# Optimization experiments

Measured on AMD Instinct MI355X. Metric: run time of the kernel, lower is better.

Reference implementation:

```python
import jax, jax.numpy as jnp
import numpy as np

N_ITERS = 100   # fixed ADMM (OSQP-style) iteration count
RHO = 1.0       # ADMM penalty
SIGMA = 1e-6    # OSQP regularization


def setup_inputs() -> dict:
    key = jax.random.key(0)
    ks = jax.random.split(key, 12)
    B, S, H, nA = 16384, 512, 1024, 24
    mEq, mIneq = 4, 8
    state = jax.random.normal(ks[0], (B, S), dtype=jnp.float32)
    Aeq = jax.random.normal(ks[1], (mEq, nA), dtype=jnp.float32)
    beq = jax.random.normal(ks[2], (mEq,), dtype=jnp.float32)
    A = jax.random.normal(ks[3], (mIneq, nA), dtype=jnp.float32)
    b = jax.random.uniform(ks[4], (mIneq,), dtype=jnp.float32)
    ub = jnp.ones((nA,), dtype=jnp.float32)
    lb = jnp.zeros((nA,), dtype=jnp.float32)
    # MLP parameters (3 Dense layers as in the flax module)
    W1 = jax.random.normal(ks[5], (S, H), dtype=jnp.float32) / np.sqrt(S).astype(np.float32)
    b1 = jnp.zeros((H,), dtype=jnp.float32)
    W2 = jax.random.normal(ks[6], (H, H), dtype=jnp.float32) / np.sqrt(H).astype(np.float32)
    b2 = jnp.zeros((H,), dtype=jnp.float32)
    W3 = jax.random.normal(ks[7], (H, nA), dtype=jnp.float32) / np.sqrt(H).astype(np.float32)
    b3 = jnp.zeros((nA,), dtype=jnp.float32)
    return dict(state=state, Aeq=Aeq, beq=beq, A=A, b=b, ub=ub, lb=lb,
                W1=W1, b1=b1, W2=W2, b2=b2, W3=W3, b3=b3)


def reference(state, Aeq, beq, A, b, ub, lb, W1, b1, W2, b2, W3, b3):
    # ---- 3-layer MLP ----
    h = jax.nn.relu(state @ W1 + b1)
    h = jax.nn.relu(h @ W2 + b2)
    raw = h @ W3 + b3                      # [B, n]
    n = raw.shape[-1]
    I = jnp.eye(n, dtype=raw.dtype)
    # ---- stack constraints exactly as solve_qp: [Aeq; A_ineq; I; -I] ----
    A_tot = jnp.concatenate([Aeq, A, I, -I], axis=0)            # [M, n]
    neg_inf = jnp.full((A.shape[0],), -jnp.inf, dtype=raw.dtype)
    l_tot = jnp.concatenate([beq, neg_inf, lb, -ub])            # [M]
    u_tot = jnp.concatenate([beq, b, ub, -lb])                  # [M]
    # ---- OSQP-style ADMM: min 0.5||x||^2 - raw'x  s.t. l <= A_tot x <= u ----
    q = -raw                                                    # [B, n]
    M = (1.0 + SIGMA) * I + RHO * (A_tot.T @ A_tot)             # [n, n] (P = I)
    Minv = jnp.linalg.inv(M)
    B_, m = q.shape[0], A_tot.shape[0]
    X0 = jnp.zeros_like(q)
    Z0 = jnp.zeros((B_, m), dtype=q.dtype)
    Y0 = jnp.zeros((B_, m), dtype=q.dtype)

    def step(carry, _):
        X, Z, Y = carry
        rhs = SIGMA * X - q + (RHO * Z - Y) @ A_tot             # [B, n]
        Xn = rhs @ Minv.T                                       # [B, n]
        Zt = Xn @ A_tot.T                                       # [B, m]
        Zn = jnp.clip(Zt + Y / RHO, l_tot, u_tot)
        Yn = Y + RHO * (Zt - Zn)
        return (Xn, Zn, Yn), None

    (X, Z, Y), _ = jax.lax.scan(step, (X0, Z0, Y0), None, length=N_ITERS)
    return X
```

## Files before the change

### kernel.cpp

```cpp
#include <hip/hip_runtime.h>

using uint = unsigned int;
using ushort = unsigned short;

typedef __attribute__((ext_vector_type(8))) short bf16x8;
typedef __attribute__((ext_vector_type(4))) float f32x4;

#define ADMM_ITERS 100
#define RHO_C 1.0f
#define SIGMA_C 1e-6f

__device__ inline ushort f2bf(float f) {
  union { float f; uint u; } c; c.f = f;
  uint u = c.u;
  uint r = (u + 0x7fffu + ((u >> 16) & 1u)) >> 16;
  return (ushort)r;
}

__device__ inline void gload_lds16(const void* g, void* l) {
  __builtin_amdgcn_global_load_lds(
      (const __attribute__((address_space(1))) void*)g,
      (__attribute__((address_space(3))) void*)l, 16, 0, 0);
}

__device__ inline void splitPack(const float* x, bf16x8& hi, bf16x8& lo) {
#pragma unroll
  for (int j = 0; j < 8; ++j) {
    uint b = __float_as_uint(x[j]);
    uint hb = b & 0xffff0000u;
    float lf = x[j] - __uint_as_float(hb);
    hi[j] = (short)(b >> 16);
    lo[j] = (short)(__float_as_uint(lf) >> 16);
  }
}

__global__ void convert_bf16(const float* __restrict__ in, ushort* __restrict__ out, int n4) {
  int i = blockIdx.x * blockDim.x + threadIdx.x;
  if (i >= n4) return;
  float4 v = ((const float4*)in)[i];
  uint2 p;
  p.x = (uint)f2bf(v.x) | ((uint)f2bf(v.y) << 16);
  p.y = (uint)f2bf(v.z) | ((uint)f2bf(v.w) << 16);
  ((uint2*)out)[i] = p;
}

__global__ void transpose_f32_bf16(const float* __restrict__ in, ushort* __restrict__ out,
                                   int R, int C, int Cout) {
  __shared__ float t[32][33];
  const int c0 = blockIdx.x * 32, r0 = blockIdx.y * 32;
  const int tx = threadIdx.x & 31, ty = threadIdx.x >> 5;
  for (int rr = ty; rr < 32; rr += 8) {
    int r = r0 + rr, c = c0 + tx;
    float v = 0.0f;
    if (r < R && c < C) v = in[(long)r * C + c];
    t[rr][tx] = v;
  }
  __syncthreads();
  for (int rr = ty; rr < 32; rr += 8) {
    int c = c0 + rr, r = r0 + tx;
    if (c < Cout && r < R) out[(long)c * R + r] = f2bf(t[tx][rr]);
  }
}

__global__ void setup_admm(const float* __restrict__ Aeq, const float* __restrict__ beq,
                           const float* __restrict__ A, const float* __restrict__ b,
                           const float* __restrict__ ub, const float* __restrict__ lb,
                           ushort* __restrict__ Th, ushort* __restrict__ Tl,
                           ushort* __restrict__ T0h, ushort* __restrict__ T0l,
                           float* __restrict__ blp, float* __restrict__ bup) {
  __shared__ float Aug[24][48];
  __shared__ float A12[12 * 24];
  __shared__ float fac[24];
  __shared__ float Tx[24][36];
  const int t = threadIdx.x;
  for (int i = t; i < 48 * 64; i += 256) { Th[i] = 0; Tl[i] = 0; }
  for (int i = t; i < 48 * 32; i += 256) { T0h[i] = 0; T0l[i] = 0; }
  if (t < 96)  A12[t] = Aeq[t];
  if (t < 192) A12[96 + t] = A[t];
  __syncthreads();
  for (int idx = t; idx < 576; idx += 256) {
    int j = idx / 24, k = idx % 24;
    float s = (j == k) ? (1.0f + SIGMA_C + 2.0f * RHO_C) : 0.0f;
    for (int r = 0; r < 12; ++r) s += RHO_C * A12[r * 24 + j] * A12[r * 24 + k];
    Aug[j][k] = s;
    Aug[j][24 + k] = (j == k) ? 1.0f : 0.0f;
  }
  __syncthreads();
  for (int p = 0; p < 24; ++p) {
    float rp = 1.0f / Aug[p][p];
    if (t < 24) fac[t] = Aug[t][p];
    __syncthreads();
    if (t < 48) Aug[p][t] *= rp;
    __syncthreads();
    for (int idx = t; idx < 24 * 48; idx += 256) {
      int r = idx / 48, c = idx % 48;
      if (r != p) Aug[r][c] -= fac[r] * Aug[p][c];
    }
    __syncthreads();
  }
  auto splitStore = [](ushort* hp, ushort* lp, int i, float v) {
    ushort hs = f2bf(v);
    float hf = __uint_as_float(((uint)hs) << 16);
    ushort ls = f2bf(v - hf);
    hp[i] = hs; lp[i] = ls;
  };
  for (int idx = t; idx < 24 * 36; idx += 256) {
    int n = idx / 36, k = idx % 36;
    float v;
    if (k < 24) v = 2.0f * Aug[n][24 + k];
    else {
      v = 0.0f;
      for (int j = 0; j < 24; ++j) v += Aug[n][24 + j] * A12[(k - 24) * 24 + j];
    }
    Tx[n][k] = v;
    splitStore(Th, Tl, n * 64 + k, v);
  }
  __syncthreads();
  for (int idx = t; idx < 12 * 36; idx += 256) {
    int m = idx / 36, k = idx % 36;
    float v = 0.0f;
    for (int j = 0; j < 24; ++j) v += A12[m * 24 + j] * Tx[j][k];
    splitStore(Th, Tl, (24 + m) * 64 + k, v);
  }
  for (int idx = t; idx < 36 * 24; idx += 256) {
    int n = idx / 24, k = idx % 24;
    float v;
    if (n < 24) v = Aug[n][24 + k];
    else {
      v = 0.0f;
      for (int j = 0; j < 24; ++j) v += A12[(n - 24) * 24 + j] * Aug[j][24 + k];
    }
    splitStore(T0h, T0l, n * 32 + k, v);
  }
  if (t < 48) {
    float lv, uv;
    if (t < 24)      { lv = lb[t]; uv = ub[t]; }
    else if (t < 28) { lv = beq[t - 24]; uv = lv; }
    else if (t < 36) { lv = -1e30f; uv = b[t - 28]; }
    else             { lv = -1e30f; uv = 1e30f; }
    blp[t] = lv; bup[t] = uv;
  }
}

template<int BM, int BN, int WM, int WN, int TM, int TN, int MODE>
__global__ __launch_bounds__(256) void gemm_bt(
    const ushort* __restrict__ A, const ushort* __restrict__ Bt,
    const float* __restrict__ bias, void* __restrict__ Cout_,
    int K, int ldc, int nvalid) {
  __shared__ char lds[(BM + BN) * 64];
  char* ldsA = lds;
  char* ldsB = lds + BM * 64;

  const int tid = threadIdx.x;
  const int wave = tid >> 6;
  const int lane = tid & 63;
  const int blockM = blockIdx.y * BM;
  const int blockN = blockIdx.x * BN;
  const int wm = (wave / WN) * (TM * 16);
  const int wn = (wave % WN) * (TN * 16);

  f32x4 acc[TM][TN] = {};

  const int l15 = lane & 15;
  const int kq = lane >> 4;
  constexpr int AI = BM / 16;
  constexpr int TOT = (BM + BN) / 16;
  const int srow = lane >> 2;
  const int kb = (lane & 3) ^ ((srow >> 1) & 3);

  for (int k0 = 0; k0 < K; k0 += 32) {
    for (int inst = wave; inst < TOT; inst += 4) {
      const bool isA = inst < AI;
      const int i = isA ? inst : inst - AI;
      const ushort* gp = (isA ? A : Bt)
          + (long)((isA ? blockM : blockN) + i * 16 + srow) * K + (k0 + kb * 8);
      char* lp = (isA ? ldsA : ldsB) + i * 1024;
      gload_lds16(gp, lp);
    }
    __syncthreads();

    bf16x8 af[TM], bfr[TN];
#pragma unroll
    for (int i = 0; i < TM; ++i) {
      int r = wm + i * 16 + l15;
      int ch = kq ^ ((r >> 1) & 3);
      af[i] = *(const bf16x8*)(ldsA + r * 64 + ch * 16);
    }
#pragma unroll
    for (int j = 0; j < TN; ++j) {
      int r = wn + j * 16 + l15;
      int ch = kq ^ ((r >> 1) & 3);
      bfr[j] = *(const bf16x8*)(ldsB + r * 64 + ch * 16);
    }
#pragma unroll
    for (int i = 0; i < TM; ++i)
#pragma unroll
      for (int j = 0; j < TN; ++j)
        acc[i][j] = __builtin_amdgcn_mfma_f32_16x16x32_bf16(af[i], bfr[j], acc[i][j], 0, 0, 0);
    __syncthreads();
  }

  const int ro = lane >> 4;
#pragma unroll
  for (int i = 0; i < TM; ++i) {
#pragma unroll
    for (int j = 0; j < TN; ++j) {
      const int col = blockN + wn + j * 16 + l15;
      float bv;
      if (MODE == 0) bv = bias[col];
      else bv = (col < nvalid) ? bias[col] : 0.0f;
#pragma unroll
      for (int r = 0; r < 4; ++r) {
        const int row = blockM + wm + i * 16 + ro * 4 + r;
        float v = acc[i][j][r] + bv;
        if (MODE == 0) {
          v = fmaxf(v, 0.0f);
          ((ushort*)Cout_)[(long)row * ldc + col] = f2bf(v);
        } else {
          if (col < nvalid) ((float*)Cout_)[(long)row * ldc + col] = v;
        }
      }
    }
  }
}

__global__ __launch_bounds__(256) void admm_mfma(
    const float* raw,
    const ushort* __restrict__ Th, const ushort* __restrict__ Tl,
    const ushort* __restrict__ T0h, const ushort* __restrict__ T0l,
    const float* __restrict__ blp, const float* __restrict__ bup,
    float* outp) {
  __shared__ __align__(16) float Ubuf[4][16][68];
  const int tid = threadIdx.x, wave = tid >> 6, lane = tid & 63;
  const int l15 = lane & 15, q = lane >> 4;
  const long rowbase = (long)blockIdx.x * 64 + wave * 16;
  float (*U)[68] = Ubuf[wave];

  for (int idx = lane; idx < 256; idx += 64)
    U[idx >> 4][48 + (idx & 15)] = 0.0f;

  float bl[3], bu[3];
#pragma unroll
  for (int t = 0; t < 3; ++t) { bl[t] = blp[16 * t + l15]; bu[t] = bup[16 * t + l15]; }

  f32x4 W[3], base[3];
  {
    bf16x8 t0h[3], t0l[3];
#pragma unroll
    for (int t = 0; t < 3; ++t) {
      t0h[t] = *(const bf16x8*)(T0h + (16 * t + l15) * 32 + q * 8);
      t0l[t] = *(const bf16x8*)(T0l + (16 * t + l15) * 32 + q * 8);
    }
    float qa[8];
    if (q < 3) {
      const float* rp = raw + (rowbase + l15) * 24 + q * 8;
      float4 v0 = *(const float4*)rp;
      float4 v1 = *(const float4*)(rp + 4);
      qa[0] = v0.x; qa[1] = v0.y; qa[2] = v0.z; qa[3] = v0.w;
      qa[4] = v1.x; qa[5] = v1.y; qa[6] = v1.z; qa[7] = v1.w;
    } else {
#pragma unroll
      for (int j = 0; j < 8; ++j) qa[j] = 0.0f;
    }
    bf16x8 qhi, qlo;
    splitPack(qa, qhi, qlo);
#pragma unroll
    for (int t = 0; t < 3; ++t) {
      f32x4 acc = {0.0f, 0.0f, 0.0f, 0.0f};
      acc = __builtin_amdgcn_mfma_f32_16x16x32_bf16(qhi, t0h[t], acc, 0, 0, 0);
      acc = __builtin_amdgcn_mfma_f32_16x16x32_bf16(qlo, t0h[t], acc, 0, 0, 0);
      acc = __builtin_amdgcn_mfma_f32_16x16x32_bf16(qhi, t0l[t], acc, 0, 0, 0);
      base[t] = acc; W[t] = acc;
    }
  }

  bf16x8 tbh[2][3], tbl[2][3];
#pragma unroll
  for (int c = 0; c < 2; ++c)
#pragma unroll
    for (int t = 0; t < 3; ++t) {
      tbh[c][t] = *(const bf16x8*)(Th + (16 * t + l15) * 64 + 32 * c + q * 8);
      tbl[c][t] = *(const bf16x8*)(Tl + (16 * t + l15) * 64 + 32 * c + q * 8);
    }

  float yb0[4], yb1[4];
#pragma unroll 1
  for (int it = 1; it < ADMM_ITERS; ++it) {
    f32x4 C[3];
#pragma unroll
    for (int t = 0; t < 3; ++t) {
#pragma unroll
      for (int r = 0; r < 4; ++r) {
        float w = W[t][r];
        float z = fminf(fmaxf(w, bl[t]), bu[t]);
        float u = 2.0f * z - w;
        float y = w - z;
        C[t][r] = base[t][r] + y;
        if (t == 0) yb0[r] = y;
        if (t == 1) yb1[r] = y;
        U[q * 4 + r][16 * t + l15] = u;
      }
    }
    bf16x8 uh[2], ul[2];
#pragma unroll
    for (int c = 0; c < 2; ++c) {
      const float* up = &U[l15][32 * c + q * 8];
      float4 a0 = *(const float4*)up;
      float4 a1 = *(const float4*)(up + 4);
      float ua[8] = {a0.x, a0.y, a0.z, a0.w, a1.x, a1.y, a1.z, a1.w};
      splitPack(ua, uh[c], ul[c]);
    }
#pragma unroll
    for (int t = 0; t < 3; ++t) {
      f32x4 acc = C[t];
#pragma unroll
      for (int c = 0; c < 2; ++c) {
        acc = __builtin_amdgcn_mfma_f32_16x16x32_bf16(uh[c], tbh[c][t], acc, 0, 0, 0);
        acc = __builtin_amdgcn_mfma_f32_16x16x32_bf16(ul[c], tbh[c][t], acc, 0, 0, 0);
        acc = __builtin_amdgcn_mfma_f32_16x16x32_bf16(uh[c], tbl[c][t], acc, 0, 0, 0);
      }
      W[t] = acc;
    }
  }

#pragma unroll
  for (int r = 0; r < 4; ++r) {
    const long row = rowbase + q * 4 + r;
    outp[row * 24 + l15] = W[0][r] - yb0[r];
    if (l15 < 8) outp[row * 24 + 16 + l15] = W[1][r] - yb1[r];
  }
}

extern "C" void kernel_launch(void* const* d_in, const int* in_sizes, int n_in,
                              void* d_out, int out_size, void* d_ws, size_t ws_size,
                              hipStream_t stream) {
  const float* state = (const float*)d_in[0];
  const float* Aeq   = (const float*)d_in[1];
  const float* beq   = (const float*)d_in[2];
  const float* Ain   = (const float*)d_in[3];
  const float* bin   = (const float*)d_in[4];
  const float* ub    = (const float*)d_in[5];
  const float* lb    = (const float*)d_in[6];
  const float* W1    = (const float*)d_in[7];
  const float* b1    = (const float*)d_in[8];
  const float* W2    = (const float*)d_in[9];
  const float* b2    = (const float*)d_in[10];
  const float* W3    = (const float*)d_in[11];
  const float* b3    = (const float*)d_in[12];

  const int Bn = in_sizes[0] / 512;
  char* ws = (char*)d_ws;
  ushort* stateB = (ushort*)(ws + 0);
  ushort* W1T    = (ushort*)(ws + 16777216);
  ushort* W2T    = (ushort*)(ws + 17825792);
  ushort* W3T    = (ushort*)(ws + 19922944);
  ushort* Th     = (ushort*)(ws + 19993600);
  ushort* Tl     = (ushort*)(ws + 19999744);
  ushort* T0h    = (ushort*)(ws + 20005888);
  ushort* T0l    = (ushort*)(ws + 20008960);
  float*  blp    = (float*) (ws + 20012032);
  float*  bup    = (float*) (ws + 20012224);
  ushort* H1     = (ushort*)(ws + 21565440);
  ushort* H2     = (ushort*)(ws + 55119872);
  float*  rawb   = (float*)d_out;

  const int n4 = (Bn * 512) / 4;
  convert_bf16<<<(n4 + 255) / 256, 256, 0, stream>>>(state, stateB, n4);
  transpose_f32_bf16<<<dim3(32, 16), 256, 0, stream>>>(W1, W1T, 512, 1024, 1024);
  transpose_f32_bf16<<<dim3(32, 32), 256, 0, stream>>>(W2, W2T, 1024, 1024, 1024);
  transpose_f32_bf16<<<dim3(1, 32),  256, 0, stream>>>(W3, W3T, 1024, 24, 32);
  setup_admm<<<1, 256, 0, stream>>>(Aeq, beq, Ain, bin, ub, lb,
                                    Th, Tl, T0h, T0l, blp, bup);

  gemm_bt<128, 128, 2, 2, 4, 4, 0><<<dim3(8, Bn / 128), 256, 0, stream>>>(
      stateB, W1T, b1, H1, 512, 1024, 1024);
  gemm_bt<128, 128, 2, 2, 4, 4, 0><<<dim3(8, Bn / 128), 256, 0, stream>>>(
      H1, W2T, b2, H2, 1024, 1024, 1024);
  gemm_bt<64, 32, 4, 1, 1, 2, 1><<<dim3(1, Bn / 64), 256, 0, stream>>>(
      H2, W3T, b3, rawb, 1024, 24, 24);

  admm_mfma<<<Bn / 64, 256, 0, stream>>>(rawb, Th, Tl, T0h, T0l, blp, bup,
                                         (float*)d_out);
}
```

Baseline: 294.9 us.

## Replace MLP layer GEMMs with 256x256-tile 8-wave pipelined MFMA kernel

Adds a new GEMM kernel for the first two MLP layers. It uses 256x256 output tiles with 8 waves, double-buffered LDS staging through global_load_lds, an XOR swizzle to avoid bank conflicts, and an XCD-aware block-index remap. The K loop is split into four phases that interleave LDS fragment reads, prefetch of the next K tile, and MFMA quads, using barriers and s_setprio to keep the matrix units busy. The goal is more data reuse per tile and better overlap of memory loads with compute. In exchange it needs 128KB of LDS per workgroup and many accumulator registers, which limits occupancy.

```diff
diff --git a/kernel.cpp b/kernel.cpp
--- a/kernel.cpp
+++ b/kernel.cpp
@@ -224,6 +224,136 @@
   }
 }
 
+#define GEMM8P_QUAD(MI0, NJ0)                                                 \
+  _Pragma("unroll") for (int mi_ = 0; mi_ < 4; ++mi_)                         \
+  _Pragma("unroll") for (int nj_ = 0; nj_ < 2; ++nj_)                         \
+  _Pragma("unroll") for (int kk_ = 0; kk_ < 2; ++kk_)                         \
+    acc[(MI0) + mi_][(NJ0) + nj_] = __builtin_amdgcn_mfma_f32_16x16x32_bf16(  \
+        aF[mi_][kk_], bF[(NJ0) + nj_][kk_], acc[(MI0) + mi_][(NJ0) + nj_],    \
+        0, 0, 0);
+
+#define GEMM8P_SYNC_PRE()                              \
+  __builtin_amdgcn_s_barrier();                        \
+  asm volatile("s_waitcnt lgkmcnt(0)" ::: "memory");   \
+  __builtin_amdgcn_sched_barrier(0);                   \
+  __builtin_amdgcn_s_setprio(1);
+
+#define GEMM8P_SYNC_POST()                             \
+  __builtin_amdgcn_s_setprio(0);                       \
+  __builtin_amdgcn_s_barrier();
+
+__global__ __launch_bounds__(512, 2) void gemm8p(
+    const ushort* __restrict__ A, const ushort* __restrict__ Bt,
+    const float* __restrict__ bias, ushort* __restrict__ Cout,
+    int K, int ldc, int nblk_n) {
+  __shared__ __align__(16) char ldsc[131072];
+
+  const int nwg = gridDim.x;
+  const int bid = blockIdx.x;
+  const int swz = (bid & 7) * (nwg >> 3) + (bid >> 3);
+  const int blockM = (swz / nblk_n) * 256;
+  const int blockN = (swz % nblk_n) * 256;
+
+  const int tid = threadIdx.x;
+  const int wave = tid >> 6;
+  const int lane = tid & 63;
+  const int l15 = lane & 15;
+  const int q = lane >> 4;
+  const int wm = (wave >> 2) * 128;
+  const int wn = (wave & 3) * 64;
+  const int nt = K >> 6;
+
+  f32x4 acc[8][4] = {};
+
+  auto stage = [&](int ts, int h) {
+    if (ts >= nt) return;
+    char* base = ldsc + ((ts & 1) << 16) + (h << 14);
+#pragma unroll
+    for (int j = 0; j < 2; ++j) {
+      const int idx = wave * 64 + j * 512 + lane;
+      const int row = idx >> 3;
+      const int cs = (idx & 7) ^ (row & 7);
+      const ushort* gp =
+          (h < 2 ? A + (long)(blockM + ((h & 1) << 7) + row) * K
+                 : Bt + (long)(blockN + ((h & 1) << 7) + row) * K)
+          + (ts << 6) + cs * 8;
+      gload_lds16(gp, base + ((wave * 64 + j * 512) << 4));
+    }
+  };
+  auto dsA = [&](int cb, int mi, int kk) {
+    const int r = wm + mi * 16 + l15;
+    const int cs = (kk * 4 + q) ^ (r & 7);
+    return *(const bf16x8*)(ldsc + (cb << 16) + r * 128 + cs * 16);
+  };
+  auto dsB = [&](int cb, int nj, int kk) {
+    const int r = wn + nj * 16 + l15;
+    const int cs = (kk * 4 + q) ^ (r & 7);
+    return *(const bf16x8*)(ldsc + (cb << 16) + 32768 + r * 128 + cs * 16);
+  };
+
+  stage(0, 0); stage(0, 1); stage(0, 2); stage(0, 3);
+  stage(1, 0);
+  asm volatile("s_waitcnt vmcnt(2)" ::: "memory");
+  __builtin_amdgcn_s_barrier();
+
+  bf16x8 aF[4][2], bF[4][2];
+#pragma unroll 1
+  for (int t = 0; t < nt; ++t) {
+    const int cb = t & 1;
+#pragma unroll
+    for (int mi = 0; mi < 4; ++mi)
+#pragma unroll
+      for (int kk = 0; kk < 2; ++kk) aF[mi][kk] = dsA(cb, mi, kk);
+#pragma unroll
+    for (int nj = 0; nj < 2; ++nj)
+#pragma unroll
+      for (int kk = 0; kk < 2; ++kk) bF[nj][kk] = dsB(cb, nj, kk);
+    stage(t + 1, 1);
+    GEMM8P_SYNC_PRE();
+    GEMM8P_QUAD(0, 0);
+    GEMM8P_SYNC_POST();
+#pragma unroll
+    for (int nj = 2; nj < 4; ++nj)
+#pragma unroll
+      for (int kk = 0; kk < 2; ++kk) bF[nj][kk] = dsB(cb, nj, kk);
+    stage(t + 1, 2);
+    GEMM8P_SYNC_PRE();
+    GEMM8P_QUAD(0, 2);
+    GEMM8P_SYNC_POST();
+#pragma unroll
+    for (int mi = 0; mi < 4; ++mi)
+#pragma unroll
+      for (int kk = 0; kk < 2; ++kk) aF[mi][kk] = dsA(cb, 4 + mi, kk);
+    stage(t + 1, 3);
+    GEMM8P_SYNC_PRE();
+    GEMM8P_QUAD(4, 2);
+    GEMM8P_SYNC_POST();
+    stage(t + 2, 0);
+    if (t + 2 < nt) { asm volatile("s_waitcnt vmcnt(2)" ::: "memory"); }
+    else            { asm volatile("s_waitcnt vmcnt(0)" ::: "memory"); }
+    __builtin_amdgcn_s_barrier();
+    __builtin_amdgcn_s_setprio(1);
+    GEMM8P_QUAD(4, 0);
+    GEMM8P_SYNC_POST();
+  }
+
+#pragma unroll
+  for (int mi = 0; mi < 8; ++mi) {
+#pragma unroll
+    for (int nj = 0; nj < 4; ++nj) {
+      const int col = blockN + wn + nj * 16 + l15;
+      const float bv = bias[col];
+#pragma unroll
+      for (int r = 0; r < 4; ++r) {
+        const int row = blockM + wm + mi * 16 + q * 4 + r;
+        float v = acc[mi][nj][r] + bv;
+        v = fmaxf(v, 0.0f);
+        Cout[(long)row * ldc + col] = f2bf(v);
+      }
+    }
+  }
+}
+
 __global__ __launch_bounds__(256) void admm_mfma(
     const float* raw,
     const ushort* __restrict__ Th, const ushort* __restrict__ Tl,
@@ -372,10 +502,10 @@
   setup_admm<<<1, 256, 0, stream>>>(Aeq, beq, Ain, bin, ub, lb,
                                     Th, Tl, T0h, T0l, blp, bup);
 
-  gemm_bt<128, 128, 2, 2, 4, 4, 0><<<dim3(8, Bn / 128), 256, 0, stream>>>(
-      stateB, W1T, b1, H1, 512, 1024, 1024);
-  gemm_bt<128, 128, 2, 2, 4, 4, 0><<<dim3(8, Bn / 128), 256, 0, stream>>>(
-      H1, W2T, b2, H2, 1024, 1024, 1024);
+  const int nblkN = 1024 / 256;
+  const int nwg = (Bn / 256) * nblkN;
+  gemm8p<<<nwg, 512, 0, stream>>>(stateB, W1T, b1, H1, 512, 1024, nblkN);
+  gemm8p<<<nwg, 512, 0, stream>>>(H1, W2T, b2, H2, 1024, 1024, nblkN);
   gemm_bt<64, 32, 4, 1, 1, 2, 1><<<dim3(1, Bn / 64), 256, 0, stream>>>(
       H2, W3T, b3, rawb, 1024, 24, 24);
 
```

Result: faster. 259.3 us (-12.1%).
